# Kernel optimization log

Measured on AMD Instinct MI355X. Metric: run time of the kernel, lower is better.

The kernel has to match this reference:

```python
import jax, jax.numpy as jnp
import numpy as np

# fixed-point config (matches init_kwargs)
DIM, H = 768, 12
DHEAD = DIM // H
DATA_W, DATA_F = 32, 16        # input activation quantizer
WQ = WK = WV = WP = (16, 8)    # weight quantizers (width, frac)
BQ = BK = BV = BP = (16, 8)    # bias quantizers
DQ = DK = DV = DS = DZ = (16, 8)  # activation quantizers after each stage
OUT_W, OUT_F = 32, 8


def qfix(x, width, frac):
    """Fixed-point integer quantizer: round to 2^-frac grid, clamp to signed width."""
    scale = jnp.float32(2.0 ** frac)
    lo = -(2.0 ** (width - 1))
    hi = 2.0 ** (width - 1) - 1
    return jnp.clip(jnp.round(x * scale), lo, hi) / scale


def setup_inputs() -> dict:
    key = jax.random.key(0)
    ks = jax.random.split(key, 5)
    return {
        "q_in": jax.random.normal(ks[0], (2, 2048, DIM), dtype=jnp.float32),
        "wqkv": jax.random.normal(ks[1], (3 * DIM, DIM), dtype=jnp.float32) * 0.05,
        "bqkv": jax.random.normal(ks[2], (3 * DIM,), dtype=jnp.float32) * 0.05,
        "wp": jax.random.normal(ks[3], (DIM, DIM), dtype=jnp.float32) * 0.05,
        "bp": jax.random.normal(ks[4], (DIM,), dtype=jnp.float32) * 0.05,
    }


def reference(q_in, wqkv, bqkv, wp, bp):
    B, N, _ = q_in.shape
    # per-head weight split: wqkv -> (H, 3*DHEAD, DIM), rows [0:d]=q, [d:2d]=k, [2d:3d]=v
    w = wqkv.reshape(H, 3 * DHEAD, DIM)
    b = bqkv.reshape(H, 3 * DHEAD)
    wq_, wk_, wv_ = w[:, :DHEAD], w[:, DHEAD:2 * DHEAD], w[:, 2 * DHEAD:]
    bq_, bk_, bv_ = b[:, :DHEAD], b[:, DHEAD:2 * DHEAD], b[:, 2 * DHEAD:]

    x = qfix(q_in, DATA_W, DATA_F)  # QuantizedLinear input quantization

    def qlin(wt, bt, wcfg, bcfg, ocfg):
        # y[b,h,n,e] = x[b,n,d] @ qw[h,e,d]^T + qb[h,e], then output quantize
        y = jnp.einsum('bnd,hed->bhne', x, qfix(wt, *wcfg)) + qfix(bt, *bcfg)[None, :, None, :]
        return qfix(y, *ocfg)

    q = qlin(wq_, bq_, WQ, BQ, DQ)  # (B,H,N,DHEAD)
    k = qlin(wk_, bk_, WK, BK, DK)
    v = qlin(wv_, bv_, WV, BV, DV)

    s = qfix(jnp.einsum('bhne,bhme->bhnm', q, k), *DS)   # (B,H,N,N) quantized scores
    z = qfix(jnp.einsum('bhnm,bhme->bhne', s, v), *DZ)   # (B,H,N,DHEAD)

    # concat heads along feature dim (torch.cat dim=2)
    zc = z.transpose(0, 2, 1, 3).reshape(B, N, DIM)

    # quantized projection: input quantized with data_z cfg (idempotent here)
    out = jnp.einsum('bnd,ed->bne', qfix(zc, *DZ), qfix(wp, *WP)) + qfix(bp, *BP)
    return qfix(out, OUT_W, OUT_F)
```

## Files before the change

### kernel.cpp

```cpp
#include <hip/hip_runtime.h>


#define NTOK 4096
#define DIM  768
#define NH   12
#define DH   64
#define SEQ  2048
#define QKVD 2304
#define NBH  24
#define LSTR 72

typedef _Float16 half8 __attribute__((ext_vector_type(8)));
typedef _Float16 half4 __attribute__((ext_vector_type(4)));
typedef __fp16   fp16x2 __attribute__((ext_vector_type(2)));
typedef float floatx4 __attribute__((ext_vector_type(4)));
typedef float floatx16 __attribute__((ext_vector_type(16)));

__global__ __launch_bounds__(256) void prep(
    const float* __restrict__ X,
    const float* __restrict__ wqkv, const float* __restrict__ bqkv,
    const float* __restrict__ wp,   const float* __restrict__ bp,
    _Float16* __restrict__ Xh, _Float16* __restrict__ Xl,
    _Float16* __restrict__ W16, _Float16* __restrict__ Wp16,
    float* __restrict__ bq24, float* __restrict__ bp16)
{
    int i = blockIdx.x * 256 + threadIdx.x;
    int i4 = i * 4;
    if (i4 < NTOK * DIM) {
        float4 x = *(const float4*)(X + i4);
        float xi[4] = {x.x, x.y, x.z, x.w};
        half4 oh, ol;
#pragma unroll
        for (int j = 0; j < 4; ++j) {
            float v = rintf(xi[j] * 65536.0f);
            float h = rintf(v * (1.0f / 2048.0f));
            ((_Float16*)&oh)[j] = (_Float16)h;
            ((_Float16*)&ol)[j] = (_Float16)(v - 2048.0f * h);
        }
        *(half4*)(Xh + i4) = oh;
        *(half4*)(Xl + i4) = ol;
    }
    if (i4 < QKVD * DIM) {
        float4 w = *(const float4*)(wqkv + i4);
        half4 o = {(_Float16)rintf(w.x * 256.0f), (_Float16)rintf(w.y * 256.0f),
                   (_Float16)rintf(w.z * 256.0f), (_Float16)rintf(w.w * 256.0f)};
        *(half4*)(W16 + i4) = o;
    }
    if (i4 < DIM * DIM) {
        float4 w = *(const float4*)(wp + i4);
        half4 o = {(_Float16)rintf(w.x * 256.0f), (_Float16)rintf(w.y * 256.0f),
                   (_Float16)rintf(w.z * 256.0f), (_Float16)rintf(w.w * 256.0f)};
        *(half4*)(Wp16 + i4) = o;
    }
    if (i < QKVD) bq24[i] = rintf(bqkv[i] * 256.0f) * 65536.0f;
    if (i < DIM)  bp16[i] = rintf(bp[i] * 256.0f) * 256.0f;
}

__global__ __launch_bounds__(256, 2) void qkv_mfma(
    const _Float16* __restrict__ Xh, const _Float16* __restrict__ Xl,
    const _Float16* __restrict__ W16, const float* __restrict__ bq24,
    _Float16* __restrict__ Q16, _Float16* __restrict__ K16,
    _Float16* __restrict__ Vt16)
{
    __shared__ __align__(16) _Float16 Ah[128 * LSTR];
    __shared__ __align__(16) _Float16 Al[128 * LSTR];
    __shared__ __align__(16) _Float16 Bs[128 * LSTR];
    const int t = threadIdx.x;
    const int w = t >> 6, lane = t & 63;
    const int l31 = lane & 31, hi = lane >> 5;
    const int m0 = blockIdx.x * 128;
    const int col0 = blockIdx.y * 128;

    floatx16 acch[4], accl[4];
#pragma unroll
    for (int ct = 0; ct < 4; ++ct)
#pragma unroll
        for (int r = 0; r < 16; ++r) { acch[ct][r] = 0.f; accl[ct][r] = 0.f; }

    for (int k0 = 0; k0 < DIM; k0 += 64) {
        __syncthreads();
#pragma unroll
        for (int i = 0; i < 4; ++i) {
            int id = t + 256 * i;
            int r = id >> 3, c8 = id & 7;
            *(half8*)(&Ah[r * LSTR + c8 * 8]) =
                *(const half8*)(Xh + (size_t)(m0 + r) * DIM + k0 + c8 * 8);
            *(half8*)(&Al[r * LSTR + c8 * 8]) =
                *(const half8*)(Xl + (size_t)(m0 + r) * DIM + k0 + c8 * 8);
            *(half8*)(&Bs[r * LSTR + c8 * 8]) =
                *(const half8*)(W16 + (size_t)(col0 + r) * DIM + k0 + c8 * 8);
        }
        __syncthreads();
#pragma unroll
        for (int i = 0; i < 4; ++i) {
            half8 ah = *(const half8*)(&Ah[(32 * w + l31) * LSTR + 16 * i + 8 * hi]);
            half8 al = *(const half8*)(&Al[(32 * w + l31) * LSTR + 16 * i + 8 * hi]);
#pragma unroll
            for (int ct = 0; ct < 4; ++ct) {
                half8 bf = *(const half8*)(&Bs[(32 * ct + l31) * LSTR + 16 * i + 8 * hi]);
                acch[ct] = __builtin_amdgcn_mfma_f32_32x32x16_f16(ah, bf, acch[ct], 0, 0, 0);
                accl[ct] = __builtin_amdgcn_mfma_f32_32x32x16_f16(al, bf, accl[ct], 0, 0, 0);
            }
        }
    }

    const int b_ = m0 >> 11;
    const int nbase = (m0 & 2047) + 32 * w;
#pragma unroll
    for (int ct = 0; ct < 4; ++ct) {
        const int c = col0 + 32 * ct + l31;
        const int h = c / 192;
        const int jj = c % 192;
        const int kind = jj >> 6;
        const int e = jj & 63;
        const int bh = b_ * NH + h;
        const float bb = bq24[c];
        float qv[16];
#pragma unroll
        for (int r = 0; r < 16; ++r) {
            float y = fmaf(2048.0f, acch[ct][r], accl[ct][r]) + bb;
            float q = rintf(y * (1.0f / 65536.0f));
            qv[r] = fminf(fmaxf(q, -32768.0f), 32767.0f);
        }
        if (kind == 2) {
#pragma unroll
            for (int g = 0; g < 4; ++g) {
                int nv = nbase + 16 * (g >> 1) + 8 * hi + 4 * (g & 1);
                half4 o = {(_Float16)qv[4 * g + 0], (_Float16)qv[4 * g + 1],
                           (_Float16)qv[4 * g + 2], (_Float16)qv[4 * g + 3]};
                *(half4*)(Vt16 + ((size_t)bh * DH + e) * SEQ + nv) = o;
            }
        } else {
            _Float16* dst = (kind == 0) ? Q16 : K16;
#pragma unroll
            for (int r = 0; r < 16; ++r) {
                int er = (r & 3) + 8 * (r >> 2) + 4 * hi;
                dst[((size_t)bh * SEQ + nbase + er) * DH + e] = (_Float16)qv[r];
            }
        }
    }
}

__global__ __launch_bounds__(256, 3) void attention_mfma(
    const _Float16* __restrict__ Q16, const _Float16* __restrict__ K16,
    const _Float16* __restrict__ Vt16,
    _Float16* __restrict__ Zh16, _Float16* __restrict__ Zl16)
{
    __shared__ __align__(16) char smem[64 * LSTR * 2 * 2];
    _Float16* Ks = (_Float16*)smem;
    _Float16* Vs = Ks + 64 * LSTR;
    float* scr = (float*)smem;

    const int t = threadIdx.x;
    const int bh = blockIdx.x;
    const int qt = blockIdx.y;
    const int w = t >> 6, lane = t & 63;
    const int l31 = lane & 31, hi = lane >> 5;
    const int wj = w & 1;
    const int wi = w >> 1;
    const _Float16* Qg = Q16 + ((size_t)bh * SEQ + qt * 64) * DH;
    const _Float16* Kg = K16 + (size_t)bh * SEQ * DH;
    const _Float16* Vg = Vt16 + (size_t)bh * DH * SEQ;

    half8 qf[4];
#pragma unroll
    for (int i = 0; i < 4; ++i)
        qf[i] = *(const half8*)(Qg + (32 * wj + l31) * DH + 16 * i + 8 * hi);

    floatx16 acc0h, acc0l, acc1h, acc1l;
#pragma unroll
    for (int r = 0; r < 16; ++r) { acc0h[r] = 0.f; acc0l[r] = 0.f; acc1h[r] = 0.f; acc1l[r] = 0.f; }

    for (int m0 = 0; m0 < SEQ; m0 += 64) {
        __syncthreads();
        {
            int r = t >> 3, k8 = t & 7;
            *(half8*)(&Ks[r * LSTR + k8 * 8]) =
                *(const half8*)(Kg + (size_t)(m0 + r) * DH + k8 * 8);
            *(half8*)(&Vs[r * LSTR + k8 * 8]) =
                *(const half8*)(Vg + (size_t)r * SEQ + m0 + k8 * 8);
            int t2 = t + 256; int r2 = t2 >> 3, k82 = t2 & 7;
            *(half8*)(&Ks[r2 * LSTR + k82 * 8]) =
                *(const half8*)(Kg + (size_t)(m0 + r2) * DH + k82 * 8);
            *(half8*)(&Vs[r2 * LSTR + k82 * 8]) =
                *(const half8*)(Vg + (size_t)r2 * SEQ + m0 + k82 * 8);
        }
        __syncthreads();

        floatx16 sc;
#pragma unroll
        for (int r = 0; r < 16; ++r) sc[r] = 0.f;
#pragma unroll
        for (int i = 0; i < 4; ++i) {
            half8 kf = *(const half8*)(&Ks[(32 * wi + l31) * LSTR + 16 * i + 8 * hi]);
            sc = __builtin_amdgcn_mfma_f32_32x32x16_f16(kf, qf[i], sc, 0, 0, 0);
        }

        float hh[16], ll[16];
#pragma unroll
        for (int r = 0; r < 16; ++r) {
            float v = rintf(sc[r] * 0.00390625f);
            v = fminf(fmaxf(v, -32768.0f), 32767.0f);
            float h = rintf(v * (1.0f / 2048.0f));
            hh[r] = h;
            ll[r] = fmaf(-2048.0f, h, v);
        }
        int dwh[4][2], dwl[4][2];
        union { fp16x2 h; int i; } cv;
#pragma unroll
        for (int g = 0; g < 4; ++g) {
            cv.h = __builtin_amdgcn_cvt_pkrtz(hh[4 * g + 0], hh[4 * g + 1]); dwh[g][0] = cv.i;
            cv.h = __builtin_amdgcn_cvt_pkrtz(hh[4 * g + 2], hh[4 * g + 3]); dwh[g][1] = cv.i;
            cv.h = __builtin_amdgcn_cvt_pkrtz(ll[4 * g + 0], ll[4 * g + 1]); dwl[g][0] = cv.i;
            cv.h = __builtin_amdgcn_cvt_pkrtz(ll[4 * g + 2], ll[4 * g + 3]); dwl[g][1] = cv.i;
        }

        half8 vf[2][2];
#pragma unroll
        for (int et = 0; et < 2; ++et)
#pragma unroll
            for (int c = 0; c < 2; ++c)
                vf[et][c] = *(const half8*)(&Vs[(32 * et + l31) * LSTR + 32 * wi + 16 * c + 8 * hi]);
#pragma unroll
        for (int c = 0; c < 2; ++c) {
            union { int b[4]; half8 v; } ubh, ubl;
            ubh.b[0] = dwh[2 * c][0];     ubh.b[1] = dwh[2 * c][1];
            ubh.b[2] = dwh[2 * c + 1][0]; ubh.b[3] = dwh[2 * c + 1][1];
            ubl.b[0] = dwl[2 * c][0];     ubl.b[1] = dwl[2 * c][1];
            ubl.b[2] = dwl[2 * c + 1][0]; ubl.b[3] = dwl[2 * c + 1][1];
            acc0h = __builtin_amdgcn_mfma_f32_32x32x16_f16(vf[0][c], ubh.v, acc0h, 0, 0, 0);
            acc0l = __builtin_amdgcn_mfma_f32_32x32x16_f16(vf[0][c], ubl.v, acc0l, 0, 0, 0);
            acc1h = __builtin_amdgcn_mfma_f32_32x32x16_f16(vf[1][c], ubh.v, acc1h, 0, 0, 0);
            acc1l = __builtin_amdgcn_mfma_f32_32x32x16_f16(vf[1][c], ubl.v, acc1l, 0, 0, 0);
        }
    }

    float zfh[16], zfl[16];
    {
        __syncthreads();
#pragma unroll
        for (int r = 0; r < 16; ++r) {
            int er = (r & 3) + 8 * (r >> 2) + 4 * hi;
            float sendh = wi ? acc0h[r] : acc1h[r];
            scr[((wj * 2 + (1 - wi)) * 32 + er) * 33 + l31] = sendh;
        }
        __syncthreads();
#pragma unroll
        for (int r = 0; r < 16; ++r) {
            int er = (r & 3) + 8 * (r >> 2) + 4 * hi;
            float keeph = wi ? acc1h[r] : acc0h[r];
            zfh[r] = keeph + scr[((wj * 2 + wi) * 32 + er) * 33 + l31];
        }
        __syncthreads();
#pragma unroll
        for (int r = 0; r < 16; ++r) {
            int er = (r & 3) + 8 * (r >> 2) + 4 * hi;
            float sendl = wi ? acc0l[r] : acc1l[r];
            scr[((wj * 2 + (1 - wi)) * 32 + er) * 33 + l31] = sendl;
        }
        __syncthreads();
#pragma unroll
        for (int r = 0; r < 16; ++r) {
            int er = (r & 3) + 8 * (r >> 2) + 4 * hi;
            float keepl = wi ? acc1l[r] : acc0l[r];
            zfl[r] = keepl + scr[((wj * 2 + wi) * 32 + er) * 33 + l31];
        }
    }

    const int b_ = bh / NH, h = bh % NH;
    const int n = qt * 64 + 32 * wj + l31;
    const size_t rowoff = ((size_t)b_ * SEQ + n) * DIM + h * DH;
#pragma unroll
    for (int g = 0; g < 4; ++g) {
        int e0 = 32 * wi + 8 * g + 4 * hi;
        half4 ph, pl;
#pragma unroll
        for (int j = 0; j < 4; ++j) {
            int r = 4 * g + j;
            float zint = fmaf(2048.0f, zfh[r], zfl[r]);
            float zq = rintf(zint * 0.00390625f);
            zq = fminf(fmaxf(zq, -32768.0f), 32767.0f);
            float zdh = rintf(zq * (1.0f / 2048.0f));
            ((_Float16*)&ph)[j] = (_Float16)zdh;
            ((_Float16*)&pl)[j] = (_Float16)(zq - 2048.0f * zdh);
        }
        *(half4*)(Zh16 + rowoff + e0) = ph;
        *(half4*)(Zl16 + rowoff + e0) = pl;
    }
}

__global__ __launch_bounds__(256) void out_mfma(
    const _Float16* __restrict__ Zh, const _Float16* __restrict__ Zl,
    const _Float16* __restrict__ Wp16, const float* __restrict__ bp16,
    float* __restrict__ O)
{
    __shared__ __align__(16) _Float16 Ah[64 * LSTR];
    __shared__ __align__(16) _Float16 Al[64 * LSTR];
    __shared__ __align__(16) _Float16 Bs[128 * LSTR];
    const int t = threadIdx.x;
    const int wave = t >> 6, lane = t & 63;
    const int lrow = lane & 15, quad = lane >> 4;
    const int m0 = blockIdx.y * 64;
    const int col0 = blockIdx.x * 128;

    floatx4 acch[4][2], accl[4][2];
#pragma unroll
    for (int fm = 0; fm < 4; ++fm)
#pragma unroll
        for (int fn = 0; fn < 2; ++fn) {
            acch[fm][fn] = (floatx4){0.f, 0.f, 0.f, 0.f};
            accl[fm][fn] = (floatx4){0.f, 0.f, 0.f, 0.f};
        }

    for (int k0 = 0; k0 < DIM; k0 += 64) {
        __syncthreads();
#pragma unroll
        for (int i = 0; i < 2; ++i) {
            int id = t + 256 * i;
            int r = id >> 3, c8 = id & 7;
            *(half8*)(&Ah[r * LSTR + c8 * 8]) =
                *(const half8*)(Zh + (size_t)(m0 + r) * DIM + k0 + c8 * 8);
            *(half8*)(&Al[r * LSTR + c8 * 8]) =
                *(const half8*)(Zl + (size_t)(m0 + r) * DIM + k0 + c8 * 8);
        }
#pragma unroll
        for (int i = 0; i < 4; ++i) {
            int id = t + 256 * i;
            int r = id >> 3, c8 = id & 7;
            *(half8*)(&Bs[r * LSTR + c8 * 8]) =
                *(const half8*)(Wp16 + (size_t)(col0 + r) * DIM + k0 + c8 * 8);
        }
        __syncthreads();
#pragma unroll
        for (int kk = 0; kk < 64; kk += 32) {
            half8 bf[2];
#pragma unroll
            for (int fn = 0; fn < 2; ++fn)
                bf[fn] = *(const half8*)(&Bs[(wave * 32 + fn * 16 + lrow) * LSTR + kk + quad * 8]);
#pragma unroll
            for (int fm = 0; fm < 4; ++fm) {
                half8 ah = *(const half8*)(&Ah[(fm * 16 + lrow) * LSTR + kk + quad * 8]);
                half8 al = *(const half8*)(&Al[(fm * 16 + lrow) * LSTR + kk + quad * 8]);
#pragma unroll
                for (int fn = 0; fn < 2; ++fn) {
                    acch[fm][fn] = __builtin_amdgcn_mfma_f32_16x16x32_f16(ah, bf[fn], acch[fm][fn], 0, 0, 0);
                    accl[fm][fn] = __builtin_amdgcn_mfma_f32_16x16x32_f16(al, bf[fn], accl[fm][fn], 0, 0, 0);
                }
            }
        }
    }

#pragma unroll
    for (int fn = 0; fn < 2; ++fn) {
        const int c = col0 + wave * 32 + fn * 16 + lrow;
        const float bb = bp16[c];
#pragma unroll
        for (int fm = 0; fm < 4; ++fm)
#pragma unroll
            for (int rg = 0; rg < 4; ++rg) {
                float y = fmaf(2048.0f, acch[fm][fn][rg], accl[fm][fn][rg]) + bb;
                float o = rintf(y * 0.00390625f) * 0.00390625f;
                int r = m0 + fm * 16 + quad * 4 + rg;
                O[(size_t)r * DIM + c] = o;
            }
    }
}

extern "C" void kernel_launch(void* const* d_in, const int* in_sizes, int n_in,
                              void* d_out, int out_size, void* d_ws, size_t ws_size,
                              hipStream_t stream) {
    const float* q_in = (const float*)d_in[0];
    const float* wqkv = (const float*)d_in[1];
    const float* bqkv = (const float*)d_in[2];
    const float* wp   = (const float*)d_in[3];
    const float* bp   = (const float*)d_in[4];

    char* w = (char*)d_ws;
    _Float16* W16  = (_Float16*)w;  w += (size_t)QKVD * DIM * 2;
    _Float16* Wp16 = (_Float16*)w;  w += (size_t)DIM * DIM * 2;
    float* bq24    = (float*)w;     w += QKVD * 4;
    float* bp16    = (float*)w;     w += DIM * 4;
    _Float16* Xh   = (_Float16*)w;  w += (size_t)NTOK * DIM * 2;
    _Float16* Xl   = (_Float16*)w;  w += (size_t)NTOK * DIM * 2;
    _Float16* Q16  = (_Float16*)w;  w += (size_t)NBH * SEQ * DH * 2;
    _Float16* K16  = (_Float16*)w;  w += (size_t)NBH * SEQ * DH * 2;
    _Float16* Vt16 = (_Float16*)w;  w += (size_t)NBH * SEQ * DH * 2;
    _Float16* Zh16 = (_Float16*)w;  w += (size_t)NTOK * DIM * 2;
    _Float16* Zl16 = (_Float16*)w;  w += (size_t)NTOK * DIM * 2;
    (void)ws_size; (void)in_sizes; (void)n_in; (void)out_size;

    prep<<<dim3(NTOK * DIM / 4 / 256), 256, 0, stream>>>(
        q_in, wqkv, bqkv, wp, bp, Xh, Xl, W16, Wp16, bq24, bp16);
    qkv_mfma<<<dim3(NTOK / 128, QKVD / 128), 256, 0, stream>>>(
        Xh, Xl, W16, bq24, Q16, K16, Vt16);
    attention_mfma<<<dim3(NBH, SEQ / 64), 256, 0, stream>>>(Q16, K16, Vt16, Zh16, Zl16);
    out_mfma<<<dim3(DIM / 128, NTOK / 64), 256, 0, stream>>>(
        Zh16, Zl16, Wp16, bp16, (float*)d_out);
}
```

Baseline: 184.9 us.

## Load MFMA operands directly from global memory instead of LDS staging

Both the QKV projection GEMM and the attention kernel stop staging tiles in shared memory behind barriers. Each lane now loads its MFMA fragments straight from global memory, relying on L1/L2 caching for reuse across waves. This removes the LDS round trips and __syncthreads stalls, but it increases global/cache traffic and exposes load latency with no explicit pipelining.

```diff
diff --git a/kernel.cpp b/kernel.cpp
--- a/kernel.cpp
+++ b/kernel.cpp
@@ -62,45 +62,31 @@
     _Float16* __restrict__ Q16, _Float16* __restrict__ K16,
     _Float16* __restrict__ Vt16)
 {
-    __shared__ __align__(16) _Float16 Ah[128 * LSTR];
-    __shared__ __align__(16) _Float16 Al[128 * LSTR];
-    __shared__ __align__(16) _Float16 Bs[128 * LSTR];
     const int t = threadIdx.x;
     const int w = t >> 6, lane = t & 63;
     const int l31 = lane & 31, hi = lane >> 5;
     const int m0 = blockIdx.x * 128;
     const int col0 = blockIdx.y * 128;
 
+    const _Float16* arow_h = Xh + (size_t)(m0 + 32 * w + l31) * DIM + 8 * hi;
+    const _Float16* arow_l = Xl + (size_t)(m0 + 32 * w + l31) * DIM + 8 * hi;
+    const _Float16* brow0 = W16 + (size_t)(col0 + l31) * DIM + 8 * hi;
+
     floatx16 acch[4], accl[4];
 #pragma unroll
     for (int ct = 0; ct < 4; ++ct)
 #pragma unroll
         for (int r = 0; r < 16; ++r) { acch[ct][r] = 0.f; accl[ct][r] = 0.f; }
 
-    for (int k0 = 0; k0 < DIM; k0 += 64) {
-        __syncthreads();
-#pragma unroll
-        for (int i = 0; i < 4; ++i) {
-            int id = t + 256 * i;
-            int r = id >> 3, c8 = id & 7;
-            *(half8*)(&Ah[r * LSTR + c8 * 8]) =
-                *(const half8*)(Xh + (size_t)(m0 + r) * DIM + k0 + c8 * 8);
-            *(half8*)(&Al[r * LSTR + c8 * 8]) =
-                *(const half8*)(Xl + (size_t)(m0 + r) * DIM + k0 + c8 * 8);
-            *(half8*)(&Bs[r * LSTR + c8 * 8]) =
-                *(const half8*)(W16 + (size_t)(col0 + r) * DIM + k0 + c8 * 8);
-        }
-        __syncthreads();
-#pragma unroll
-        for (int i = 0; i < 4; ++i) {
-            half8 ah = *(const half8*)(&Ah[(32 * w + l31) * LSTR + 16 * i + 8 * hi]);
-            half8 al = *(const half8*)(&Al[(32 * w + l31) * LSTR + 16 * i + 8 * hi]);
-#pragma unroll
-            for (int ct = 0; ct < 4; ++ct) {
-                half8 bf = *(const half8*)(&Bs[(32 * ct + l31) * LSTR + 16 * i + 8 * hi]);
-                acch[ct] = __builtin_amdgcn_mfma_f32_32x32x16_f16(ah, bf, acch[ct], 0, 0, 0);
-                accl[ct] = __builtin_amdgcn_mfma_f32_32x32x16_f16(al, bf, accl[ct], 0, 0, 0);
-            }
+#pragma unroll 2
+    for (int k0 = 0; k0 < DIM; k0 += 16) {
+        half8 ah = *(const half8*)(arow_h + k0);
+        half8 al = *(const half8*)(arow_l + k0);
+#pragma unroll
+        for (int ct = 0; ct < 4; ++ct) {
+            half8 bf = *(const half8*)(brow0 + (size_t)(32 * ct) * DIM + k0);
+            acch[ct] = __builtin_amdgcn_mfma_f32_32x32x16_f16(ah, bf, acch[ct], 0, 0, 0);
+            accl[ct] = __builtin_amdgcn_mfma_f32_32x32x16_f16(al, bf, accl[ct], 0, 0, 0);
         }
     }
 
@@ -146,10 +132,7 @@
     const _Float16* __restrict__ Vt16,
     _Float16* __restrict__ Zh16, _Float16* __restrict__ Zl16)
 {
-    __shared__ __align__(16) char smem[64 * LSTR * 2 * 2];
-    _Float16* Ks = (_Float16*)smem;
-    _Float16* Vs = Ks + 64 * LSTR;
-    float* scr = (float*)smem;
+    __shared__ float scr[4 * 32 * 33];
 
     const int t = threadIdx.x;
     const int bh = blockIdx.x;
@@ -167,32 +150,20 @@
     for (int i = 0; i < 4; ++i)
         qf[i] = *(const half8*)(Qg + (32 * wj + l31) * DH + 16 * i + 8 * hi);
 
+    const _Float16* krow = Kg + (size_t)(32 * wi + l31) * DH + 8 * hi;
+    const _Float16* vrow0 = Vg + (size_t)l31 * SEQ + 32 * wi + 8 * hi;
+
     floatx16 acc0h, acc0l, acc1h, acc1l;
 #pragma unroll
     for (int r = 0; r < 16; ++r) { acc0h[r] = 0.f; acc0l[r] = 0.f; acc1h[r] = 0.f; acc1l[r] = 0.f; }
 
     for (int m0 = 0; m0 < SEQ; m0 += 64) {
-        __syncthreads();
-        {
-            int r = t >> 3, k8 = t & 7;
-            *(half8*)(&Ks[r * LSTR + k8 * 8]) =
-                *(const half8*)(Kg + (size_t)(m0 + r) * DH + k8 * 8);
-            *(half8*)(&Vs[r * LSTR + k8 * 8]) =
-                *(const half8*)(Vg + (size_t)r * SEQ + m0 + k8 * 8);
-            int t2 = t + 256; int r2 = t2 >> 3, k82 = t2 & 7;
-            *(half8*)(&Ks[r2 * LSTR + k82 * 8]) =
-                *(const half8*)(Kg + (size_t)(m0 + r2) * DH + k82 * 8);
-            *(half8*)(&Vs[r2 * LSTR + k82 * 8]) =
-                *(const half8*)(Vg + (size_t)r2 * SEQ + m0 + k82 * 8);
-        }
-        __syncthreads();
-
         floatx16 sc;
 #pragma unroll
         for (int r = 0; r < 16; ++r) sc[r] = 0.f;
 #pragma unroll
         for (int i = 0; i < 4; ++i) {
-            half8 kf = *(const half8*)(&Ks[(32 * wi + l31) * LSTR + 16 * i + 8 * hi]);
+            half8 kf = *(const half8*)(krow + (size_t)m0 * DH + 16 * i);
             sc = __builtin_amdgcn_mfma_f32_32x32x16_f16(kf, qf[i], sc, 0, 0, 0);
         }
 
@@ -215,23 +186,19 @@
             cv.h = __builtin_amdgcn_cvt_pkrtz(ll[4 * g + 2], ll[4 * g + 3]); dwl[g][1] = cv.i;
         }
 
-        half8 vf[2][2];
-#pragma unroll
-        for (int et = 0; et < 2; ++et)
-#pragma unroll
-            for (int c = 0; c < 2; ++c)
-                vf[et][c] = *(const half8*)(&Vs[(32 * et + l31) * LSTR + 32 * wi + 16 * c + 8 * hi]);
 #pragma unroll
         for (int c = 0; c < 2; ++c) {
+            half8 vf0 = *(const half8*)(vrow0 + m0 + 16 * c);
+            half8 vf1 = *(const half8*)(vrow0 + (size_t)32 * SEQ + m0 + 16 * c);
             union { int b[4]; half8 v; } ubh, ubl;
             ubh.b[0] = dwh[2 * c][0];     ubh.b[1] = dwh[2 * c][1];
             ubh.b[2] = dwh[2 * c + 1][0]; ubh.b[3] = dwh[2 * c + 1][1];
             ubl.b[0] = dwl[2 * c][0];     ubl.b[1] = dwl[2 * c][1];
             ubl.b[2] = dwl[2 * c + 1][0]; ubl.b[3] = dwl[2 * c + 1][1];
-            acc0h = __builtin_amdgcn_mfma_f32_32x32x16_f16(vf[0][c], ubh.v, acc0h, 0, 0, 0);
-            acc0l = __builtin_amdgcn_mfma_f32_32x32x16_f16(vf[0][c], ubl.v, acc0l, 0, 0, 0);
-            acc1h = __builtin_amdgcn_mfma_f32_32x32x16_f16(vf[1][c], ubh.v, acc1h, 0, 0, 0);
-            acc1l = __builtin_amdgcn_mfma_f32_32x32x16_f16(vf[1][c], ubl.v, acc1l, 0, 0, 0);
+            acc0h = __builtin_amdgcn_mfma_f32_32x32x16_f16(vf0, ubh.v, acc0h, 0, 0, 0);
+            acc0l = __builtin_amdgcn_mfma_f32_32x32x16_f16(vf0, ubl.v, acc0l, 0, 0, 0);
+            acc1h = __builtin_amdgcn_mfma_f32_32x32x16_f16(vf1, ubh.v, acc1h, 0, 0, 0);
+            acc1l = __builtin_amdgcn_mfma_f32_32x32x16_f16(vf1, ubl.v, acc1l, 0, 0, 0);
         }
     }
 
```

After: 292.0 us. 1.58x slower.
